# Kernel tuning notes

Measured on AMD Instinct MI355X. Metric: run time of the kernel, lower is better.

The kernel has to match this reference:

```python
import jax, jax.numpy as jnp
import numpy as np

E = 1024
FF = 4096
B, S = 4, 2048
EPS = 1e-5

def _layernorm(x, g, b):
    m = jnp.mean(x, axis=-1, keepdims=True)
    v = jnp.var(x, axis=-1, keepdims=True)
    return (x - m) * jax.lax.rsqrt(v + EPS) * g + b

def setup_inputs() -> dict:
    key = jax.random.key(0)
    ks = jax.random.split(key, 16)
    def lin(k, fan_in, shape):
        bound = 1.0 / np.sqrt(fan_in)
        return jax.random.uniform(k, shape, jnp.float32, -bound, bound)
    return {
        "src_embs": jax.random.normal(ks[0], (B, S, E), jnp.float32),
        "Wq_w": lin(ks[1], E, (E, E)), "Wq_b": lin(ks[2], E, (E,)),
        "Wk_w": lin(ks[3], E, (E, E)), "Wk_b": lin(ks[4], E, (E,)),
        "Wv_w": lin(ks[5], E, (E, E)), "Wv_b": lin(ks[6], E, (E,)),
        "Wo_w": lin(ks[7], E, (E, E)), "Wo_b": lin(ks[8], E, (E,)),
        "W1_w": lin(ks[9], E, (FF, E)), "W1_b": lin(ks[10], E, (FF,)),
        "W2_w": lin(ks[11], FF, (E, FF)), "W2_b": lin(ks[12], FF, (E,)),
        "g1": jnp.ones((E,), jnp.float32), "b1": jnp.zeros((E,), jnp.float32),
        "g2": jnp.ones((E,), jnp.float32), "b2": jnp.zeros((E,), jnp.float32),
        "g3": jnp.ones((E,), jnp.float32), "b3": jnp.zeros((E,), jnp.float32),
    }

def reference(src_embs, Wq_w, Wq_b, Wk_w, Wk_b, Wv_w, Wv_b, Wo_w, Wo_b,
              W1_w, W1_b, W2_w, W2_b, g1, b1, g2, b2, g3, b3):
    x = _layernorm(src_embs, g1, b1)
    Q = x @ Wq_w.T + Wq_b
    K = x @ Wk_w.T + Wk_b
    V = x @ Wv_w.T + Wv_b
    # single-head attention, scaled by sqrt(embed_dim) per source
    scores = jnp.einsum('bqe,bke->bqk', Q, K) / jnp.sqrt(jnp.float32(E))
    attn = jax.nn.softmax(scores, axis=-1)
    attn_out = jnp.einsum('bqk,bke->bqe', attn, V) @ Wo_w.T + Wo_b
    h = src_embs + attn_out
    hn = _layernorm(h, g2, b2)
    ff = jax.nn.relu(hn @ W1_w.T + W1_b) @ W2_w.T + W2_b
    out = h + ff
    return _layernorm(out, g3, b3)
```

## Files before the change

### kernel.cpp

```cpp
#include <hip/hip_runtime.h>
#include <cstdint>
#include <cmath>

#define E_DIM 1024
#define FF_DIM 4096
#define B_DIM 4
#define S_DIM 2048
#define NTOK (B_DIM * S_DIM)
#define QKV_N 3072

typedef __bf16 bf16;
typedef __attribute__((ext_vector_type(8))) __bf16 bf16x8;
typedef __attribute__((ext_vector_type(4))) float f32x4;

__device__ __forceinline__ void gload_lds16(const void* g, void* l) {
  __builtin_amdgcn_global_load_lds(
      (const __attribute__((address_space(1))) unsigned int*)g,
      (__attribute__((address_space(3))) unsigned int*)l, 16, 0, 0);
}

__device__ __forceinline__ float waveRedSum(float v) {
#pragma unroll
  for (int o = 32; o > 0; o >>= 1) v += __shfl_xor(v, o, 64);
  return v;
}
__device__ __forceinline__ float waveRedMax(float v) {
#pragma unroll
  for (int o = 32; o > 0; o >>= 1) v = fmaxf(v, __shfl_xor(v, o, 64));
  return v;
}

__global__ __launch_bounds__(256) void cvt_k(const float* __restrict__ in,
                                             bf16* __restrict__ out, int n4) {
  int i = blockIdx.x * 256 + threadIdx.x;
  if (i < n4) {
    float4 v = reinterpret_cast<const float4*>(in)[i];
    bf16* o = out + (size_t)i * 4;
    o[0] = (bf16)v.x; o[1] = (bf16)v.y; o[2] = (bf16)v.z; o[3] = (bf16)v.w;
  }
}

template <typename OutT>
__global__ __launch_bounds__(256) void layernorm_k(const float* __restrict__ x,
                                                   OutT* __restrict__ out,
                                                   const float* __restrict__ g,
                                                   const float* __restrict__ b) {
  const int row = blockIdx.x;
  const int tid = threadIdx.x;
  const float4 v = reinterpret_cast<const float4*>(x + (size_t)row * E_DIM)[tid];
  float s = v.x + v.y + v.z + v.w;
  float q = v.x * v.x + v.y * v.y + v.z * v.z + v.w * v.w;
  s = waveRedSum(s);
  q = waveRedSum(q);
  __shared__ float sa[4], sb[4];
  const int lane = tid & 63, wid = tid >> 6;
  if (lane == 0) { sa[wid] = s; sb[wid] = q; }
  __syncthreads();
  s = sa[0] + sa[1] + sa[2] + sa[3];
  q = sb[0] + sb[1] + sb[2] + sb[3];
  const float mean = s * (1.0f / E_DIM);
  const float var = q * (1.0f / E_DIM) - mean * mean;
  const float rstd = rsqrtf(var + 1e-5f);
  const int c = tid * 4;
  OutT* op = out + (size_t)row * E_DIM + c;
  const float vv[4] = {v.x, v.y, v.z, v.w};
#pragma unroll
  for (int j = 0; j < 4; ++j)
    op[j] = (OutT)((vv[j] - mean) * rstd * g[c + j] + b[c + j]);
}

__global__ __launch_bounds__(256) void softmax_k(bf16* __restrict__ scores) {
  const int row = blockIdx.x;
  bf16* rp = scores + (size_t)row * S_DIM;
  const int tid = threadIdx.x;
  const int lane = tid & 63, wid = tid >> 6;
  bf16x8 v8 = *reinterpret_cast<const bf16x8*>(rp + tid * 8);
  float v[8];
#pragma unroll
  for (int j = 0; j < 8; ++j) v[j] = (float)v8[j];
  float mx = v[0];
#pragma unroll
  for (int j = 1; j < 8; ++j) mx = fmaxf(mx, v[j]);
  mx = waveRedMax(mx);
  __shared__ float sm_[4], ss_[4];
  if (lane == 0) sm_[wid] = mx;
  __syncthreads();
  mx = fmaxf(fmaxf(sm_[0], sm_[1]), fmaxf(sm_[2], sm_[3]));
  float e[8];
  float s = 0.f;
#pragma unroll
  for (int j = 0; j < 8; ++j) { e[j] = __expf(v[j] - mx); s += e[j]; }
  s = waveRedSum(s);
  if (lane == 0) ss_[wid] = s;
  __syncthreads();
  s = ss_[0] + ss_[1] + ss_[2] + ss_[3];
  const float inv = 1.0f / s;
  bf16x8 o;
#pragma unroll
  for (int j = 0; j < 8; ++j) o[j] = (bf16)(e[j] * inv);
  *reinterpret_cast<bf16x8*>(rp + tid * 8) = o;
}

__global__ __launch_bounds__(256) void transpose_k(const bf16* __restrict__ in,
                                                   int ld_in, size_t bstride_in,
                                                   bf16* __restrict__ out) {
  __shared__ bf16 t[32][33];
  const int b = blockIdx.z;
  const bf16* ip = in + (size_t)b * bstride_in;
  bf16* op = out + (size_t)b * S_DIM * E_DIM;
  const int e0 = blockIdx.x * 32, s0 = blockIdx.y * 32;
  const int tx = threadIdx.x & 31, ty = threadIdx.x >> 5;
#pragma unroll
  for (int r = 0; r < 32; r += 8)
    t[ty + r][tx] = ip[(size_t)(s0 + ty + r) * ld_in + e0 + tx];
  __syncthreads();
#pragma unroll
  for (int r = 0; r < 32; r += 8)
    op[(size_t)(e0 + ty + r) * S_DIM + s0 + tx] = t[tx][ty + r];
}

template <int BN, typename OutT, bool RELU>
__global__ __launch_bounds__(512) void gemm8p_k(
    const bf16* __restrict__ A0, int lda, const bf16* __restrict__ Bt0, int ldb,
    OutT* __restrict__ C0, int ldc, int M, int N, int K,
    const float* __restrict__ bias, const float* __restrict__ resid, int ldr,
    float scale, size_t sAz, size_t sBz, size_t sCz) {
  constexpr int BM = 256;
  constexpr int WAVE_N = BN / 4;
  constexpr int NPH = (BN == 256) ? 4 : 2;
  constexpr int NHH = (BN == 256) ? 2 : 1;
  constexpr int NCH_B = BN / 64;
  constexpr int NCH = 4 + NCH_B;
  constexpr int CPP = NCH / NPH;
  constexpr int DEPTH = (BN == 256) ? 2 : 3;
  constexpr int DBUF = (BM + BN) * 128;
  __shared__ __align__(16) char smem[DEPTH * DBUF];

  const int tid = threadIdx.x;
  const int lane = tid & 63;
  const int wid = tid >> 6;
  const int wr = wid >> 2;
  const int wc = wid & 3;

  const bf16* A = A0 + (size_t)blockIdx.z * sAz;
  const bf16* Bt = Bt0 + (size_t)blockIdx.z * sBz;
  OutT* C = C0 + (size_t)blockIdx.z * sCz;

  const int gx = gridDim.x;
  const int nwg = gx * gridDim.y;
  int wg = blockIdx.y * gx + blockIdx.x;
  {
    const int q = nwg >> 3, r8 = nwg & 7;
    const int xcd = wg & 7, lin = wg >> 3;
    wg = (xcd < r8 ? xcd * (q + 1) : r8 * (q + 1) + (xcd - r8) * q) + lin;
  }
  const int m0 = (wg / gx) * 256;
  const int n0 = (wg % gx) * BN;

  auto stage_chunk = [&](int t, int c) {
    char* base = smem + (t % DEPTH) * DBUF;
    const int r8 = tid >> 3;
    const int gg = tid & 7;
    if (c < NCH_B) {
      const int row = c * 64 + r8;
      const int g = gg ^ (row & 7);
      gload_lds16(Bt + (size_t)(n0 + row) * ldb + t * 64 + g * 8,
                  base + BM * 128 + c * 8192 + wid * 1024);
    } else {
      const int i = c - NCH_B;
      const int ca = ((i & 1) << 1) | (i >> 1);
      const int row = ca * 64 + r8;
      const int g = gg ^ (row & 7);
      gload_lds16(A + (size_t)(m0 + row) * lda + t * 64 + g * 8,
                  base + ca * 8192 + wid * 1024);
    }
  };

  f32x4 acc[2][4][NHH][2] = {};
  bf16x8 af[4][2];
  bf16x8 bfv[NHH][2][2];

  const int NT = K >> 6;
  if constexpr (BN == 256) {
#pragma unroll
    for (int c = 0; c < NCH; ++c) stage_chunk(0, c);
    asm volatile("s_waitcnt vmcnt(2)" ::: "memory");
  } else {
#pragma unroll
    for (int c = 0; c < NCH; ++c) stage_chunk(0, c);
#pragma unroll
    for (int c = 0; c < NCH; ++c) stage_chunk(1, c);
    asm volatile("s_waitcnt vmcnt(6)" ::: "memory");
  }
  __builtin_amdgcn_s_barrier();

  for (int t = 0; t < NT; ++t) {
    const char* lA = smem + (t % DEPTH) * DBUF;
    const char* lB = lA + BM * 128;
#pragma unroll
    for (int p = 0; p < NPH; ++p) {
      const int mh = (BN == 256) ? (p >> 1) : p;
      const int nh = (BN == 256) ? (p & 1) : 0;
      if ((BN == 256) ? (p == 0 || p == 2) : true) {
#pragma unroll
        for (int fm = 0; fm < 4; ++fm) {
          const int row = wr * 128 + mh * 64 + fm * 16 + (lane & 15);
#pragma unroll
          for (int ks = 0; ks < 2; ++ks) {
            const int g = ((ks << 2) | (lane >> 4)) ^ (row & 7);
            af[fm][ks] = *reinterpret_cast<const bf16x8*>(lA + row * 128 + g * 16);
          }
        }
      }
      if (p < NHH) {
#pragma unroll
        for (int fn = 0; fn < 2; ++fn) {
          const int row = wc * WAVE_N + p * 32 + fn * 16 + (lane & 15);
#pragma unroll
          for (int ks = 0; ks < 2; ++ks) {
            const int g = ((ks << 2) | (lane >> 4)) ^ (row & 7);
            bfv[p][fn][ks] =
                *reinterpret_cast<const bf16x8*>(lB + row * 128 + g * 16);
          }
        }
      }
      if constexpr (BN == 256) {
        if (t + 1 < NT) {
#pragma unroll
          for (int c = 0; c < CPP; ++c) stage_chunk(t + 1, p * CPP + c);
        }
      } else {
        if (t + 2 < NT) {
#pragma unroll
          for (int c = 0; c < CPP; ++c) stage_chunk(t + 2, p * CPP + c);
        }
      }
      __builtin_amdgcn_s_barrier();
      __builtin_amdgcn_s_setprio(1);
#pragma unroll
      for (int fm = 0; fm < 4; ++fm)
#pragma unroll
        for (int fn = 0; fn < 2; ++fn) {
          acc[mh][fm][nh][fn] = __builtin_amdgcn_mfma_f32_16x16x32_bf16(
              af[fm][0], bfv[nh][fn][0], acc[mh][fm][nh][fn], 0, 0, 0);
          acc[mh][fm][nh][fn] = __builtin_amdgcn_mfma_f32_16x16x32_bf16(
              af[fm][1], bfv[nh][fn][1], acc[mh][fm][nh][fn], 0, 0, 0);
        }
      __builtin_amdgcn_s_setprio(0);
      if constexpr (BN == 256) {
        if (p == 1) {
          if (t + 1 < NT) asm volatile("s_waitcnt vmcnt(4)" ::: "memory");
          else            asm volatile("s_waitcnt vmcnt(0)" ::: "memory");
        }
        if (p == NPH - 1) {
          asm volatile("s_waitcnt vmcnt(2)" ::: "memory");
        }
      } else {
        if (p == NPH - 1) {
          if (t + 2 < NT) asm volatile("s_waitcnt vmcnt(6)" ::: "memory");
          else            asm volatile("s_waitcnt vmcnt(0)" ::: "memory");
        }
      }
      __builtin_amdgcn_s_barrier();
    }
  }

#pragma unroll
  for (int mh = 0; mh < 2; ++mh)
#pragma unroll
    for (int nh = 0; nh < NHH; ++nh)
#pragma unroll
      for (int fn = 0; fn < 2; ++fn) {
        const int col = n0 + wc * WAVE_N + nh * 32 + fn * 16 + (lane & 15);
        const float bv = bias ? bias[col] : 0.0f;
#pragma unroll
        for (int fm = 0; fm < 4; ++fm)
#pragma unroll
          for (int i = 0; i < 4; ++i) {
            const int row = m0 + wr * 128 + mh * 64 + fm * 16 + (lane >> 4) * 4 + i;
            float v = acc[mh][fm][nh][fn][i] * scale + bv;
            if (resid) v += resid[(size_t)row * ldr + col];
            if (RELU) v = fmaxf(v, 0.0f);
            C[(size_t)row * ldc + col] = (OutT)v;
          }
      }
}

extern "C" void kernel_launch(void* const* d_in, const int* in_sizes, int n_in,
                              void* d_out, int out_size, void* d_ws,
                              size_t ws_size, hipStream_t stream) {
  const float* src = (const float*)d_in[0];
  const float* Wq_w = (const float*)d_in[1];
  const float* Wq_b = (const float*)d_in[2];
  const float* Wk_w = (const float*)d_in[3];
  const float* Wk_b = (const float*)d_in[4];
  const float* Wv_w = (const float*)d_in[5];
  const float* Wv_b = (const float*)d_in[6];
  const float* Wo_w = (const float*)d_in[7];
  const float* Wo_b = (const float*)d_in[8];
  const float* W1_w = (const float*)d_in[9];
  const float* W1_b = (const float*)d_in[10];
  const float* W2_w = (const float*)d_in[11];
  const float* W2_b = (const float*)d_in[12];
  const float* g1 = (const float*)d_in[13];
  const float* b1 = (const float*)d_in[14];
  const float* g2 = (const float*)d_in[15];
  const float* b2 = (const float*)d_in[16];
  const float* g3 = (const float*)d_in[17];
  const float* b3 = (const float*)d_in[18];
  float* out = (float*)d_out;
  (void)ws_size; (void)in_sizes; (void)n_in; (void)out_size;

  const size_t MB = 1ull << 20;
  char* ws = (char*)d_ws;
  bf16* wqkv = (bf16*)(ws + 0 * MB);
  bf16* wo = (bf16*)(ws + 6 * MB);
  bf16* w1 = (bf16*)(ws + 8 * MB);
  bf16* w2 = (bf16*)(ws + 16 * MB);
  bf16* Cqkv = (bf16*)(ws + 24 * MB);
  bf16* Vt = (bf16*)(ws + 72 * MB);
  bf16* scoresB = (bf16*)(ws + 88 * MB);
  bf16* xln = (bf16*)(ws + 88 * MB);
  float* bqkv = (float*)(ws + 104 * MB);
  bf16* ctx = Cqkv;
  bf16* hn = scoresB;
  bf16* f1 = (bf16*)(ws + 24 * MB);
  float* h = out;

  cvt_k<<<(E_DIM * E_DIM / 4 + 255) / 256, 256, 0, stream>>>(Wq_w, wqkv, E_DIM * E_DIM / 4);
  cvt_k<<<(E_DIM * E_DIM / 4 + 255) / 256, 256, 0, stream>>>(Wk_w, wqkv + (size_t)E_DIM * E_DIM, E_DIM * E_DIM / 4);
  cvt_k<<<(E_DIM * E_DIM / 4 + 255) / 256, 256, 0, stream>>>(Wv_w, wqkv + 2 * (size_t)E_DIM * E_DIM, E_DIM * E_DIM / 4);
  cvt_k<<<(E_DIM * E_DIM / 4 + 255) / 256, 256, 0, stream>>>(Wo_w, wo, E_DIM * E_DIM / 4);
  cvt_k<<<(FF_DIM * E_DIM / 4 + 255) / 256, 256, 0, stream>>>(W1_w, w1, FF_DIM * E_DIM / 4);
  cvt_k<<<(FF_DIM * E_DIM / 4 + 255) / 256, 256, 0, stream>>>(W2_w, w2, FF_DIM * E_DIM / 4);
  hipMemcpyAsync(bqkv, Wq_b, E_DIM * 4, hipMemcpyDeviceToDevice, stream);
  hipMemcpyAsync(bqkv + E_DIM, Wk_b, E_DIM * 4, hipMemcpyDeviceToDevice, stream);
  hipMemcpyAsync(bqkv + 2 * E_DIM, Wv_b, E_DIM * 4, hipMemcpyDeviceToDevice, stream);

  layernorm_k<bf16><<<NTOK, 256, 0, stream>>>(src, xln, g1, b1);

  dim3 gQKV(QKV_N / 256, NTOK / 256);
  gemm8p_k<256, bf16, false><<<gQKV, 512, 0, stream>>>(
      xln, E_DIM, wqkv, E_DIM, Cqkv, QKV_N, NTOK, QKV_N, E_DIM,
      bqkv, nullptr, 0, 1.0f, 0, 0, 0);

  dim3 gSc(S_DIM / 256, S_DIM / 256, B_DIM);
  gemm8p_k<256, bf16, false><<<gSc, 512, 0, stream>>>(
      Cqkv, QKV_N, Cqkv + E_DIM, QKV_N, scoresB, S_DIM, S_DIM, S_DIM, E_DIM,
      nullptr, nullptr, 0, 1.0f / 32.0f,
      (size_t)S_DIM * QKV_N, (size_t)S_DIM * QKV_N, (size_t)S_DIM * S_DIM);

  softmax_k<<<B_DIM * S_DIM, 256, 0, stream>>>(scoresB);

  transpose_k<<<dim3(E_DIM / 32, S_DIM / 32, B_DIM), 256, 0, stream>>>(
      Cqkv + 2 * E_DIM, QKV_N, (size_t)S_DIM * QKV_N, Vt);

  dim3 gPV(E_DIM / 128, S_DIM / 256, B_DIM);
  gemm8p_k<128, bf16, false><<<gPV, 512, 0, stream>>>(
      scoresB, S_DIM, Vt, S_DIM, ctx, E_DIM, S_DIM, E_DIM, S_DIM,
      nullptr, nullptr, 0, 1.0f,
      (size_t)S_DIM * S_DIM, (size_t)S_DIM * E_DIM, (size_t)S_DIM * E_DIM);

  dim3 gWo(E_DIM / 128, NTOK / 256);
  gemm8p_k<128, float, false><<<gWo, 512, 0, stream>>>(
      ctx, E_DIM, wo, E_DIM, h, E_DIM, NTOK, E_DIM, E_DIM,
      Wo_b, src, E_DIM, 1.0f, 0, 0, 0);

  layernorm_k<bf16><<<NTOK, 256, 0, stream>>>(h, hn, g2, b2);

  dim3 gF1(FF_DIM / 256, NTOK / 256);
  gemm8p_k<256, bf16, true><<<gF1, 512, 0, stream>>>(
      hn, E_DIM, w1, E_DIM, f1, FF_DIM, NTOK, FF_DIM, E_DIM,
      W1_b, nullptr, 0, 1.0f, 0, 0, 0);

  dim3 gF2(E_DIM / 128, NTOK / 256);
  gemm8p_k<128, float, false><<<gF2, 512, 0, stream>>>(
      f1, FF_DIM, w2, FF_DIM, out, E_DIM, NTOK, E_DIM, FF_DIM,
      W2_b, h, E_DIM, 1.0f, 0, 0, 0);

  layernorm_k<float><<<NTOK, 256, 0, stream>>>(out, out, g3, b3);
}
```

Baseline: 416.9 us.

## Remap BN=128 GEMM warps to 4x2 grid and use 256-wide tiles for FFN2

For the BN=128 variant, the 8 waves are rearranged from a 2x4 grid (each wave 128x32) to a 4x2 grid (each wave 64x64). Each k-phase now loads 4 A and 4 B fragments per wave, so LDS read traffic per MFMA drops. The FFN down-projection also moves to the BN=256 variant, which doubles B-tile reuse but halves the grid to 128 blocks. That smaller grid can leave compute units idle on a 256-CU part.

```diff
diff --git a/kernel.cpp b/kernel.cpp
--- a/kernel.cpp
+++ b/kernel.cpp
@@ -126,9 +126,7 @@
     const float* __restrict__ bias, const float* __restrict__ resid, int ldr,
     float scale, size_t sAz, size_t sBz, size_t sCz) {
   constexpr int BM = 256;
-  constexpr int WAVE_N = BN / 4;
   constexpr int NPH = (BN == 256) ? 4 : 2;
-  constexpr int NHH = (BN == 256) ? 2 : 1;
   constexpr int NCH_B = BN / 64;
   constexpr int NCH = 4 + NCH_B;
   constexpr int CPP = NCH / NPH;
@@ -139,8 +137,6 @@
   const int tid = threadIdx.x;
   const int lane = tid & 63;
   const int wid = tid >> 6;
-  const int wr = wid >> 2;
-  const int wc = wid & 3;
 
   const bf16* A = A0 + (size_t)blockIdx.z * sAz;
   const bf16* Bt = Bt0 + (size_t)blockIdx.z * sBz;
@@ -176,9 +172,8 @@
     }
   };
 
-  f32x4 acc[2][4][NHH][2] = {};
-  bf16x8 af[4][2];
-  bf16x8 bfv[NHH][2][2];
+  f32x4 accQ[2][4][2][2] = {};
+  f32x4 accH[4][4] = {};
 
   const int NT = K >> 6;
   if constexpr (BN == 256) {
@@ -197,93 +192,141 @@
   for (int t = 0; t < NT; ++t) {
     const char* lA = smem + (t % DEPTH) * DBUF;
     const char* lB = lA + BM * 128;
-#pragma unroll
-    for (int p = 0; p < NPH; ++p) {
-      const int mh = (BN == 256) ? (p >> 1) : p;
-      const int nh = (BN == 256) ? (p & 1) : 0;
-      if ((BN == 256) ? (p == 0 || p == 2) : true) {
-#pragma unroll
-        for (int fm = 0; fm < 4; ++fm) {
-          const int row = wr * 128 + mh * 64 + fm * 16 + (lane & 15);
-#pragma unroll
-          for (int ks = 0; ks < 2; ++ks) {
-            const int g = ((ks << 2) | (lane >> 4)) ^ (row & 7);
-            af[fm][ks] = *reinterpret_cast<const bf16x8*>(lA + row * 128 + g * 16);
+    if constexpr (BN == 256) {
+      const int wr = wid >> 2;
+      const int wc = wid & 3;
+      bf16x8 af[4][2];
+      bf16x8 bfv[2][2][2];
+#pragma unroll
+      for (int p = 0; p < 4; ++p) {
+        const int mh = p >> 1, nh = p & 1;
+        if (p == 0 || p == 2) {
+#pragma unroll
+          for (int fm = 0; fm < 4; ++fm) {
+            const int row = wr * 128 + mh * 64 + fm * 16 + (lane & 15);
+#pragma unroll
+            for (int ks = 0; ks < 2; ++ks) {
+              const int g = ((ks << 2) | (lane >> 4)) ^ (row & 7);
+              af[fm][ks] = *reinterpret_cast<const bf16x8*>(lA + row * 128 + g * 16);
+            }
           }
         }
-      }
-      if (p < NHH) {
-#pragma unroll
-        for (int fn = 0; fn < 2; ++fn) {
-          const int row = wc * WAVE_N + p * 32 + fn * 16 + (lane & 15);
-#pragma unroll
-          for (int ks = 0; ks < 2; ++ks) {
-            const int g = ((ks << 2) | (lane >> 4)) ^ (row & 7);
-            bfv[p][fn][ks] =
-                *reinterpret_cast<const bf16x8*>(lB + row * 128 + g * 16);
+        if (p < 2) {
+#pragma unroll
+          for (int fn = 0; fn < 2; ++fn) {
+            const int row = wc * 64 + p * 32 + fn * 16 + (lane & 15);
+#pragma unroll
+            for (int ks = 0; ks < 2; ++ks) {
+              const int g = ((ks << 2) | (lane >> 4)) ^ (row & 7);
+              bfv[p][fn][ks] =
+                  *reinterpret_cast<const bf16x8*>(lB + row * 128 + g * 16);
+            }
           }
         }
-      }
-      if constexpr (BN == 256) {
         if (t + 1 < NT) {
 #pragma unroll
-          for (int c = 0; c < CPP; ++c) stage_chunk(t + 1, p * CPP + c);
-        }
-      } else {
-        if (t + 2 < NT) {
-#pragma unroll
-          for (int c = 0; c < CPP; ++c) stage_chunk(t + 2, p * CPP + c);
-        }
-      }
-      __builtin_amdgcn_s_barrier();
-      __builtin_amdgcn_s_setprio(1);
-#pragma unroll
-      for (int fm = 0; fm < 4; ++fm)
-#pragma unroll
-        for (int fn = 0; fn < 2; ++fn) {
-          acc[mh][fm][nh][fn] = __builtin_amdgcn_mfma_f32_16x16x32_bf16(
-              af[fm][0], bfv[nh][fn][0], acc[mh][fm][nh][fn], 0, 0, 0);
-          acc[mh][fm][nh][fn] = __builtin_amdgcn_mfma_f32_16x16x32_bf16(
-              af[fm][1], bfv[nh][fn][1], acc[mh][fm][nh][fn], 0, 0, 0);
-        }
-      __builtin_amdgcn_s_setprio(0);
-      if constexpr (BN == 256) {
+          for (int c = 0; c < 2; ++c) stage_chunk(t + 1, p * 2 + c);
+        }
+        __builtin_amdgcn_s_barrier();
+        __builtin_amdgcn_s_setprio(1);
+#pragma unroll
+        for (int fm = 0; fm < 4; ++fm)
+#pragma unroll
+          for (int fn = 0; fn < 2; ++fn) {
+            accQ[mh][fm][nh][fn] = __builtin_amdgcn_mfma_f32_16x16x32_bf16(
+                af[fm][0], bfv[nh][fn][0], accQ[mh][fm][nh][fn], 0, 0, 0);
+            accQ[mh][fm][nh][fn] = __builtin_amdgcn_mfma_f32_16x16x32_bf16(
+                af[fm][1], bfv[nh][fn][1], accQ[mh][fm][nh][fn], 0, 0, 0);
+          }
+        __builtin_amdgcn_s_setprio(0);
         if (p == 1) {
           if (t + 1 < NT) asm volatile("s_waitcnt vmcnt(4)" ::: "memory");
           else            asm volatile("s_waitcnt vmcnt(0)" ::: "memory");
         }
-        if (p == NPH - 1) {
+        if (p == 3) {
           asm volatile("s_waitcnt vmcnt(2)" ::: "memory");
         }
-      } else {
-        if (p == NPH - 1) {
+        __builtin_amdgcn_s_barrier();
+      }
+    } else {
+      const int wr = wid >> 1;
+      const int wc = wid & 1;
+#pragma unroll
+      for (int p = 0; p < 2; ++p) {
+        bf16x8 af[4], bf[4];
+#pragma unroll
+        for (int fm = 0; fm < 4; ++fm) {
+          const int row = wr * 64 + fm * 16 + (lane & 15);
+          const int g = ((p << 2) | (lane >> 4)) ^ (row & 7);
+          af[fm] = *reinterpret_cast<const bf16x8*>(lA + row * 128 + g * 16);
+        }
+#pragma unroll
+        for (int fn = 0; fn < 4; ++fn) {
+          const int row = wc * 64 + fn * 16 + (lane & 15);
+          const int g = ((p << 2) | (lane >> 4)) ^ (row & 7);
+          bf[fn] = *reinterpret_cast<const bf16x8*>(lB + row * 128 + g * 16);
+        }
+        if (t + 2 < NT) {
+#pragma unroll
+          for (int c = 0; c < 3; ++c) stage_chunk(t + 2, p * 3 + c);
+        }
+        __builtin_amdgcn_s_barrier();
+        __builtin_amdgcn_s_setprio(1);
+#pragma unroll
+        for (int fm = 0; fm < 4; ++fm)
+#pragma unroll
+          for (int fn = 0; fn < 4; ++fn)
+            accH[fm][fn] = __builtin_amdgcn_mfma_f32_16x16x32_bf16(
+                af[fm], bf[fn], accH[fm][fn], 0, 0, 0);
+        __builtin_amdgcn_s_setprio(0);
+        if (p == 1) {
           if (t + 2 < NT) asm volatile("s_waitcnt vmcnt(6)" ::: "memory");
           else            asm volatile("s_waitcnt vmcnt(0)" ::: "memory");
         }
+        __builtin_amdgcn_s_barrier();
       }
-      __builtin_amdgcn_s_barrier();
     }
   }
 
-#pragma unroll
-  for (int mh = 0; mh < 2; ++mh)
-#pragma unroll
-    for (int nh = 0; nh < NHH; ++nh)
-#pragma unroll
-      for (int fn = 0; fn < 2; ++fn) {
-        const int col = n0 + wc * WAVE_N + nh * 32 + fn * 16 + (lane & 15);
-        const float bv = bias ? bias[col] : 0.0f;
-#pragma unroll
-        for (int fm = 0; fm < 4; ++fm)
-#pragma unroll
-          for (int i = 0; i < 4; ++i) {
-            const int row = m0 + wr * 128 + mh * 64 + fm * 16 + (lane >> 4) * 4 + i;
-            float v = acc[mh][fm][nh][fn][i] * scale + bv;
-            if (resid) v += resid[(size_t)row * ldr + col];
-            if (RELU) v = fmaxf(v, 0.0f);
-            C[(size_t)row * ldc + col] = (OutT)v;
-          }
-      }
+  if constexpr (BN == 256) {
+    const int wr = wid >> 2, wc = wid & 3;
+#pragma unroll
+    for (int mh = 0; mh < 2; ++mh)
+#pragma unroll
+      for (int nh = 0; nh < 2; ++nh)
+#pragma unroll
+        for (int fn = 0; fn < 2; ++fn) {
+          const int col = n0 + wc * 64 + nh * 32 + fn * 16 + (lane & 15);
+          const float bv = bias ? bias[col] : 0.0f;
+#pragma unroll
+          for (int fm = 0; fm < 4; ++fm)
+#pragma unroll
+            for (int i = 0; i < 4; ++i) {
+              const int row = m0 + wr * 128 + mh * 64 + fm * 16 + (lane >> 4) * 4 + i;
+              float v = accQ[mh][fm][nh][fn][i] * scale + bv;
+              if (resid) v += resid[(size_t)row * ldr + col];
+              if (RELU) v = fmaxf(v, 0.0f);
+              C[(size_t)row * ldc + col] = (OutT)v;
+            }
+        }
+  } else {
+    const int wr = wid >> 1, wc = wid & 1;
+#pragma unroll
+    for (int fn = 0; fn < 4; ++fn) {
+      const int col = n0 + wc * 64 + fn * 16 + (lane & 15);
+      const float bv = bias ? bias[col] : 0.0f;
+#pragma unroll
+      for (int fm = 0; fm < 4; ++fm)
+#pragma unroll
+        for (int i = 0; i < 4; ++i) {
+          const int row = m0 + wr * 64 + fm * 16 + (lane >> 4) * 4 + i;
+          float v = accH[fm][fn][i] * scale + bv;
+          if (resid) v += resid[(size_t)row * ldr + col];
+          if (RELU) v = fmaxf(v, 0.0f);
+          C[(size_t)row * ldc + col] = (OutT)v;
+        }
+    }
+  }
 }
 
 extern "C" void kernel_launch(void* const* d_in, const int* in_sizes, int n_in,
@@ -373,8 +416,8 @@
       hn, E_DIM, w1, E_DIM, f1, FF_DIM, NTOK, FF_DIM, E_DIM,
       W1_b, nullptr, 0, 1.0f, 0, 0, 0);
 
-  dim3 gF2(E_DIM / 128, NTOK / 256);
-  gemm8p_k<128, float, false><<<gF2, 512, 0, stream>>>(
+  dim3 gF2(E_DIM / 256, NTOK / 256);
+  gemm8p_k<256, float, false><<<gF2, 512, 0, stream>>>(
       f1, FF_DIM, w2, FF_DIM, out, E_DIM, NTOK, E_DIM, FF_DIM,
       W2_b, h, E_DIM, 1.0f, 0, 0, 0);
 
```

Result: slower. 461.2 us (+10.6%).
